# Kernel optimization log

Hardware: AMD Instinct MI355X
Metric: run time of the kernel (lower is better)

## Reference

```python
import jax, jax.numpy as jnp
import numpy as np

N, G, D, A = 131072, 256, 256, 64
NEG = -1e9
EPS = 1e-10


def segment_softmax(logits, idx, num_segments):
    # numerically stable softmax over ragged segments; works for [N] and [N, A]
    m = jax.ops.segment_max(logits, idx, num_segments=num_segments)
    e = jnp.exp(logits - m[idx])
    s = jax.ops.segment_sum(e, idx, num_segments=num_segments)
    return e / s[idx]


def setup_inputs() -> dict:
    key = jax.random.key(0)
    ks = jax.random.split(key, 12)
    values = jax.random.normal(ks[0], (N, D), dtype=jnp.float32)
    indices = jnp.sort(jax.random.randint(ks[1], (N,), 0, G))
    a_action = jax.random.randint(ks[2], (G,), 0, A)
    a_node = jax.random.randint(ks[3], (G,), 0, N)
    action_mask = jax.random.randint(ks[4], (G, A), 0, 2).astype(bool)
    n_nodes = jax.ops.segment_sum(jnp.ones((N,), jnp.int32), indices, num_segments=G)
    s = 0.02
    w_node = jax.random.normal(ks[5], (D,), dtype=jnp.float32) * s          # node_prob (no bias)
    W_agn = jax.random.normal(ks[6], (A, D), dtype=jnp.float32) * s         # action_given_node_prob
    b_agn = jnp.zeros((A,), jnp.float32)
    W_nga = jax.random.normal(ks[7], (A, D), dtype=jnp.float32) * s         # node_given_action_prob
    b_nga = jnp.zeros((A,), jnp.float32)
    W_qna = jax.random.normal(ks[8], (A, D), dtype=jnp.float32) * s         # q_node__action
    b_qna = jnp.zeros((A,), jnp.float32)
    W_qan = jax.random.normal(ks[9], (A, D), dtype=jnp.float32) * s         # q_action__node
    b_qan = jnp.zeros((A,), jnp.float32)
    return {"values": values, "indices": indices, "a_action": a_action, "a_node": a_node,
            "action_mask": action_mask, "n_nodes": n_nodes,
            "w_node": w_node, "W_agn": W_agn, "b_agn": b_agn, "W_nga": W_nga, "b_nga": b_nga,
            "W_qna": W_qna, "b_qna": b_qna, "W_qan": W_qan, "b_qan": b_qan}


def reference(values, indices, a_action, a_node, action_mask, n_nodes,
              w_node, W_agn, b_agn, W_nga, b_nga, W_qna, b_qna, W_qan, b_qan):
    n_g = action_mask.shape[0]
    segsum = lambda x: jax.ops.segment_sum(x, indices, num_segments=n_g)

    node_logits = values @ w_node                         # [N]
    agn_logits = values @ W_agn.T + b_agn                 # [N, A] action_given_node
    nga_logits = values @ W_nga.T + b_nga                 # [N, A] node_given_action
    mask_actions = action_mask[indices]                   # [N, A] per-node action validity

    # p(n) per graph, p(a|n) per node, p(a) per graph by marginalization
    p_n = segment_softmax(node_logits, indices, n_g)                       # [N]
    p_a_given_n = jax.nn.softmax(jnp.where(mask_actions, agn_logits, NEG), axis=-1)  # [N, A]
    p_a = segsum(p_n[:, None] * p_a_given_n)                               # [G, A]

    # masked p(n|a) used for eval (logprob/entropy)
    p_n_a_masked = segment_softmax(jnp.where(mask_actions, nga_logits, NEG), indices, n_g)  # [N, A]

    g_ar = jnp.arange(n_g)
    logprob = jnp.log(p_a[g_ar, a_action] + EPS) + jnp.log(p_n_a_masked[a_node, a_action] + EPS)  # [G]

    H_a = -jnp.sum(p_a * jnp.log(p_a + EPS), axis=-1)                      # [G]
    H_n_given_a = -segsum(p_n_a_masked * jnp.log(p_n_a_masked + EPS))      # [G, A]
    entropy = H_a + jnp.sum(p_a * H_n_given_a, axis=-1)                    # [G]

    # value estimate (unmasked p_n__a, as in f())
    p_n__a = segment_softmax(nga_logits, indices, n_g)                     # [N, A]
    q_a = segsum(values @ W_qan.T + b_qan)                                 # [G, A]
    q_n__a = values @ W_qna.T + b_qna                                      # [N, A]
    value = jnp.sum(p_a * (q_a + segsum(p_n__a * q_n__a)), axis=-1)        # [G]

    return (logprob, entropy, value, p_a, p_n__a)
```

## Files before the change

kernel.cpp:

```cpp
#include <hip/hip_runtime.h>
#include <hip/hip_bf16.h>

typedef unsigned short u16;
typedef unsigned int u32;
typedef __attribute__((ext_vector_type(4))) float f32x4;
typedef __attribute__((ext_vector_type(8))) short s16x8;
typedef __attribute__((ext_vector_type(8))) unsigned short u16x8;
typedef __attribute__((ext_vector_type(4))) unsigned short u16x4;

#define EPS_V (1e-10f)
#define TILES 4
#define NHALF (TILES * 4)

__device__ __forceinline__ u16 f2bf(float f) {
  unsigned u = __float_as_uint(f);
  u += 0x7fffu + ((u >> 16) & 1u);
  return (u16)(u >> 16);
}
__device__ __forceinline__ float bf2f(u16 h) {
  return __uint_as_float(((unsigned)h) << 16);
}
__device__ __forceinline__ float wred_sum(float v) {
#pragma unroll
  for (int o = 32; o; o >>= 1) v += __shfl_xor(v, o);
  return v;
}
__device__ __forceinline__ float red16(float v) {
  v += __shfl_xor(v, 1); v += __shfl_xor(v, 2);
  v += __shfl_xor(v, 4); v += __shfl_xor(v, 8);
  return v;
}
__device__ __forceinline__ bool mask_at(const void* m, int kind, int idx) {
  if (kind == 0) return ((const int*)m)[idx] != 0;
  if (kind == 1) return ((const float*)m)[idx] != 0.0f;
  return ((const unsigned char*)m)[idx] != 0;
}

__global__ __launch_bounds__(256) void k0_fused(
    const int* __restrict__ n_nodes, const unsigned int* __restrict__ mask_raw,
    const float* __restrict__ w_node, const float* __restrict__ W_agn,
    const float* __restrict__ W_nga, const float* __restrict__ W_qna,
    const float* __restrict__ W_qan,
    int* __restrict__ seg_start, int* __restrict__ mkind,
    float* __restrict__ zero_base, int nzero, u16* __restrict__ Wpack,
    int G, int ndw) {
  const int b = blockIdx.x;
  const int t = threadIdx.x;
  if (b == 0) {
    if (t < 64) {
      int base = t * 4;
      int v0 = (base + 0 < G) ? n_nodes[base + 0] : 0;
      int v1 = (base + 1 < G) ? n_nodes[base + 1] : 0;
      int v2 = (base + 2 < G) ? n_nodes[base + 2] : 0;
      int v3 = (base + 3 < G) ? n_nodes[base + 3] : 0;
      int lsum = v0 + v1 + v2 + v3;
      int x = lsum;
#pragma unroll
      for (int o = 1; o < 64; o <<= 1) {
        int y = __shfl_up(x, o);
        if (t >= o) x += y;
      }
      int run = x - lsum;
      if (base + 0 < G) seg_start[base + 0] = run; run += v0;
      if (base + 1 < G) seg_start[base + 1] = run; run += v1;
      if (base + 2 < G) seg_start[base + 2] = run; run += v2;
      if (base + 3 < G) seg_start[base + 3] = run; run += v3;
      if (t == 63) seg_start[G] = run;
    }
  } else if (b == 1) {
    __shared__ int notInt, notFloat;
    if (t == 0) { notInt = 0; notFloat = 0; }
    __syncthreads();
    int li = 0, lf = 0;
    for (int i = t; i < ndw; i += 256) {
      unsigned v = mask_raw[i];
      if (v != 0u && v != 1u) li = 1;
      if (v != 0u && v != 0x3F800000u) lf = 1;
    }
    if (li) atomicOr(&notInt, 1);
    if (lf) atomicOr(&notFloat, 1);
    __syncthreads();
    if (t == 0) mkind[0] = (!notInt) ? 0 : ((!notFloat) ? 1 : 2);
  } else if (b < 2 + 80) {
    int q = (b - 2) * 256 + t;
    int col = q >> 6, k = (q & 63) * 4;
    f32x4 v = (f32x4){0.f, 0.f, 0.f, 0.f};
    if (col < 64) v = *reinterpret_cast<const f32x4*>(W_agn + col * 256 + k);
    else if (col < 128) v = *reinterpret_cast<const f32x4*>(W_nga + (col - 64) * 256 + k);
    else if (col < 192) v = *reinterpret_cast<const f32x4*>(W_qna + (col - 128) * 256 + k);
    else if (col < 256) v = *reinterpret_cast<const f32x4*>(W_qan + (col - 192) * 256 + k);
    else if (col == 256) v = *reinterpret_cast<const f32x4*>(w_node + k);
    u16x4 h;
    h[0] = f2bf(v[0]); h[1] = f2bf(v[1]); h[2] = f2bf(v[2]); h[3] = f2bf(v[3]);
    *reinterpret_cast<u16x4*>(Wpack + (size_t)q * 4) = h;
  } else {
    int idx = (b - 82) * 256 + t;
    if (idx < nzero) zero_base[idx] = 0.f;
  }
}

__device__ __forceinline__ s16x8 frag_from_lds(const float* Vf, int m, int k0) {
  int g0 = ((k0 >> 2) ^ (m & 7));
  int g1 = g0 ^ 1;
  const f32x4 lo = *reinterpret_cast<const f32x4*>(&Vf[m * 256 + g0 * 4]);
  const f32x4 hi = *reinterpret_cast<const f32x4*>(&Vf[m * 256 + g1 * 4]);
  union { s16x8 v; u32 u[4]; } r;
  r.u[0] = __builtin_amdgcn_perm(__float_as_uint(lo[1]), __float_as_uint(lo[0]), 0x07060302u);
  r.u[1] = __builtin_amdgcn_perm(__float_as_uint(lo[3]), __float_as_uint(lo[2]), 0x07060302u);
  r.u[2] = __builtin_amdgcn_perm(__float_as_uint(hi[1]), __float_as_uint(hi[0]), 0x07060302u);
  r.u[3] = __builtin_amdgcn_perm(__float_as_uint(hi[3]), __float_as_uint(hi[2]), 0x07060302u);
  return r.v;
}

__global__ __launch_bounds__(256, 2) void k1_gemm(
    const float* __restrict__ values, const u16* __restrict__ Wpack,
    const int* __restrict__ indices, const void* __restrict__ mask,
    const int* __restrict__ mkind,
    const float* __restrict__ b_agn, const float* __restrict__ b_nga,
    const float* __restrict__ b_qna, const float* __restrict__ b_qan,
    u16* __restrict__ nga_bf, float* __restrict__ nga_f32,
    u16* __restrict__ qna, float* __restrict__ q_a,
    float* __restrict__ pa_un, float* __restrict__ Sn_at, int nga_is_bf) {
  __shared__ float ring[4][16 * 256];
  __shared__ u16 outbuf[2][16][68];
  __shared__ int segid[TILES * 64];

  const int t = threadIdx.x;
  const int lane = t & 63;
  const int wave = t >> 6;
  const int ln15 = lane & 15;
  const int kg = lane >> 4;
  const int blk0 = blockIdx.x * (TILES * 64);
  const int kind = mkind[0];

  s16x8 bfr[4][8];
  {
    const u16* wb = Wpack + (size_t)(wave * 64 + ln15) * 256 + kg * 8;
#pragma unroll
    for (int cg = 0; cg < 4; ++cg)
#pragma unroll
      for (int s = 0; s < 8; ++s)
        bfr[cg][s] = *reinterpret_cast<const s16x8*>(wb + (size_t)(cg * 16) * 256 + s * 32);
  }
  float bias_c[4];
  {
    const float* bp = (wave == 0) ? b_agn : (wave == 1) ? b_nga
                    : (wave == 2) ? b_qna : b_qan;
#pragma unroll
    for (int cg = 0; cg < 4; ++cg) bias_c[cg] = bp[cg * 16 + ln15];
  }
  s16x8 bn[8];
  if (wave == 0) {
    const u16* wb = Wpack + (size_t)(256 + ln15) * 256 + kg * 8;
#pragma unroll
    for (int s = 0; s < 8; ++s)
      bn[s] = *reinterpret_cast<const s16x8*>(wb + s * 32);
  }
  if (wave == 3) {
#pragma unroll
    for (int j = 0; j < 4; ++j)
      segid[lane + 64 * j] = indices[blk0 + lane + 64 * j];
  }
  float qpart[4] = {0.f, 0.f, 0.f, 0.f};
  int qg = (wave == 3) ? segid[kg * 4] : 0;
  float pa_[4] = {0.f, 0.f, 0.f, 0.f};
  float sn_ = 0.f;
  int pg = 0;
  bool mv[4] = {false, false, false, false};
  if (wave == 0) {
    pg = indices[blk0 + kg * 4];
#pragma unroll
    for (int cg = 0; cg < 4; ++cg)
      mv[cg] = mask_at(mask, kind, pg * 64 + cg * 16 + ln15);
  }

#define STAGE(hh)                                                              \
  {                                                                            \
    float* dst_ = ring[(hh) & 3];                                              \
    const int r0_ = blk0 + (hh) * 16;                                          \
    _Pragma("unroll")                                                          \
    for (int i_ = 0; i_ < 4; ++i_) {                                           \
      int m_ = wave * 4 + i_;                                                  \
      const float* gp_ = values + (size_t)(r0_ + m_) * 256 + ((lane ^ (m_ & 7)) << 2); \
      __builtin_amdgcn_global_load_lds(                                        \
          (const __attribute__((address_space(1))) void*)gp_,                  \
          (__attribute__((address_space(3))) void*)&dst_[m_ * 256], 16, 0, 0); \
    }                                                                          \
  }

  STAGE(0);
  STAGE(1);

  for (int h = 0; h < NHALF; ++h) {
    if (h + 2 < NHALF) STAGE(h + 2);
    if (h == 0) {
      asm volatile("s_waitcnt vmcnt(8) lgkmcnt(0)" ::: "memory");
    } else if (!nga_is_bf && wave == 1) {
      asm volatile("s_waitcnt vmcnt(0)" ::: "memory");
    } else if (h == NHALF - 1) {
      asm volatile("s_waitcnt vmcnt(0)" ::: "memory");
    } else if (h == NHALF - 2) {
      if (wave == 1 || wave == 2) asm volatile("s_waitcnt vmcnt(8)" ::: "memory");
      else                        asm volatile("s_waitcnt vmcnt(4)" ::: "memory");
    } else {
      if (wave == 1 || wave == 2) asm volatile("s_waitcnt vmcnt(12)" ::: "memory");
      else                        asm volatile("s_waitcnt vmcnt(8)" ::: "memory");
    }
    __builtin_amdgcn_sched_barrier(0);
    __builtin_amdgcn_s_barrier();
    __builtin_amdgcn_sched_barrier(0);

    const float* buf = ring[h & 3];
    const int row0 = blk0 + h * 16;

    f32x4 acc[4];
#pragma unroll
    for (int cg = 0; cg < 4; ++cg) acc[cg] = (f32x4){0.f, 0.f, 0.f, 0.f};
    f32x4 an0 = (f32x4){0.f, 0.f, 0.f, 0.f};

#pragma unroll
    for (int s = 0; s < 8; ++s) {
      const int k0 = s * 32 + kg * 8;
      s16x8 a0 = frag_from_lds(buf, ln15, k0);
#pragma unroll
      for (int cg = 0; cg < 4; ++cg)
        acc[cg] = __builtin_amdgcn_mfma_f32_16x16x32_bf16(a0, bfr[cg][s], acc[cg], 0, 0, 0);
      if (wave == 0)
        an0 = __builtin_amdgcn_mfma_f32_16x16x32_bf16(a0, bn[s], an0, 0, 0, 0);
    }

    if (wave == 0) {
#pragma unroll
      for (int r = 0; r < 4; ++r) {
        int m = kg * 4 + r;
        int g = segid[h * 16 + m];
        if (g != pg) {
#pragma unroll
          for (int cg = 0; cg < 4; ++cg) {
            atomicAdd(&pa_un[pg * 64 + cg * 16 + ln15], pa_[cg]);
            pa_[cg] = 0.f;
          }
          if (ln15 == 0) atomicAdd(&Sn_at[pg], sn_);
          sn_ = 0.f;
          pg = g;
#pragma unroll
          for (int cg = 0; cg < 4; ++cg)
            mv[cg] = mask_at(mask, kind, pg * 64 + cg * 16 + ln15);
        }
        float e0[4];
        float rs = 0.f;
#pragma unroll
        for (int cg = 0; cg < 4; ++cg) {
          e0[cg] = mv[cg] ? __expf(acc[cg][r] + bias_c[cg]) : 0.f;
          rs += e0[cg];
        }
        rs = red16(rs);
        float pn_e = __shfl(__expf(an0[r]), kg * 16);
        if (ln15 == 0) sn_ += pn_e;
        if (rs > 0.f) {
          float inv = pn_e / rs;
#pragma unroll
          for (int cg = 0; cg < 4; ++cg) pa_[cg] += e0[cg] * inv;
        } else {
#pragma unroll
          for (int cg = 0; cg < 4; ++cg) pa_[cg] += pn_e * 0.015625f;
        }
      }
    } else if (wave == 3) {
#pragma unroll
      for (int r = 0; r < 4; ++r) {
        int m = kg * 4 + r;
        int g = segid[h * 16 + m];
        if (g != qg) {
#pragma unroll
          for (int cg = 0; cg < 4; ++cg) {
            atomicAdd(&q_a[qg * 64 + cg * 16 + ln15], qpart[cg]);
            qpart[cg] = 0.f;
          }
          qg = g;
        }
#pragma unroll
        for (int cg = 0; cg < 4; ++cg)
          qpart[cg] += acc[cg][r] + bias_c[cg];
      }
    } else if (wave == 1 && !nga_is_bf) {
#pragma unroll
      for (int r = 0; r < 4; ++r)
#pragma unroll
        for (int cg = 0; cg < 4; ++cg)
          nga_f32[(size_t)(row0 + kg * 4 + r) * 64 + cg * 16 + ln15] = acc[cg][r] + bias_c[cg];
    } else {
#pragma unroll
      for (int r = 0; r < 4; ++r) {
        int m = kg * 4 + r;
#pragma unroll
        for (int cg = 0; cg < 4; ++cg)
          outbuf[wave - 1][m][cg * 16 + ln15] = f2bf(acc[cg][r] + bias_c[cg]);
      }
      u16* dstp = (wave == 1) ? nga_bf : qna;
#pragma unroll
      for (int j = 0; j < 4; ++j) {
        int li = lane + j * 64;
        int rr = li >> 4, cc = (li & 15) * 4;
        u16x4 v = *reinterpret_cast<const u16x4*>(&outbuf[wave - 1][rr][cc]);
        *reinterpret_cast<u16x4*>(dstp + (size_t)row0 * 64 + (size_t)li * 4) = v;
      }
    }
  }
#undef STAGE

  if (wave == 3) {
#pragma unroll
    for (int cg = 0; cg < 4; ++cg)
      atomicAdd(&q_a[qg * 64 + cg * 16 + ln15], qpart[cg]);
  }
  if (wave == 0) {
#pragma unroll
    for (int cg = 0; cg < 4; ++cg)
      atomicAdd(&pa_un[pg * 64 + cg * 16 + ln15], pa_[cg]);
    if (ln15 == 0) atomicAdd(&Sn_at[pg], sn_);
  }
}

__global__ __launch_bounds__(1024) void k2_segment(
    const u16* __restrict__ nga_bf, float* __restrict__ nga_f32,
    const u16* __restrict__ qna, const int* __restrict__ seg_start,
    const void* __restrict__ mask, const int* __restrict__ mkind,
    const float* __restrict__ q_a, const float* __restrict__ pa_un,
    const float* __restrict__ Sn_at,
    float* __restrict__ p_a, float* __restrict__ entropy, float* __restrict__ value,
    float* __restrict__ Su, float* __restrict__ pna, int nga_is_bf) {
  const int g = blockIdx.x;
  const int s = seg_start[g], e = seg_start[g + 1];
  const int n = e - s;
  const int t = threadIdx.x, lane = t & 63, wave = t >> 6;

  __shared__ float cs[16][64], cv[16][64], ci[16][64];
  __shared__ float sS[64];

  float s_u = 0.f, v_u = 0.f, i_u = 0.f;
  for (int i = s + wave; i < e; i += 16) {
    size_t base = (size_t)i * 64 + lane;
    float y = nga_is_bf ? bf2f(nga_bf[base]) : nga_f32[base];
    float ey = __expf(y);
    s_u += ey;
    v_u += ey * y;
    i_u += ey * bf2f(qna[base]);
  }
  cs[wave][lane] = s_u; cv[wave][lane] = v_u; ci[wave][lane] = i_u;
  __syncthreads();

  const int kind = mkind[0];
  if (t < 64) {
    int a = t;
    float S = 0.f, V = 0.f, I = 0.f;
#pragma unroll
    for (int w = 0; w < 16; ++w) { S += cs[w][a]; V += cv[w][a]; I += ci[w][a]; }
    float Sn = Sn_at[g];
    float P = (Sn > 0.f) ? pa_un[g * 64 + a] / Sn : 0.f;
    p_a[g * 64 + a] = P;
    Su[g * 64 + a] = S;
    sS[a] = (S > 0.f) ? 1.f / S : 0.f;
    float inner = (S > 0.f) ? I / S : 0.f;
    float Q = q_a[g * 64 + a];
    bool mva = mask_at(mask, kind, g * 64 + a);
    float Hn;
    if (n <= 0) Hn = 0.f;
    else if (!mva) Hn = -logf(1.0f / (float)n + EPS_V);
    else Hn = (S > 0.f) ? (logf(S) - V / S) : 0.f;
    float ent_c = -P * logf(P + EPS_V) + P * Hn;
    float val_c = P * (Q + inner);
    ent_c = wred_sum(ent_c);
    val_c = wred_sum(val_c);
    if (a == 0) { entropy[g] = ent_c; value[g] = val_c; }
  }
  __syncthreads();

  const int a0 = (t & 7) * 8;
  float is0 = sS[a0 + 0], is1 = sS[a0 + 1], is2 = sS[a0 + 2], is3 = sS[a0 + 3];
  float is4 = sS[a0 + 4], is5 = sS[a0 + 5], is6 = sS[a0 + 6], is7 = sS[a0 + 7];
  for (int i = s + (t >> 3); i < e; i += 128) {
    size_t base = (size_t)i * 64 + a0;
    float4 o0, o1;
    if (nga_is_bf) {
      u16x8 y = *reinterpret_cast<const u16x8*>(nga_bf + base);
      o0.x = __expf(bf2f(y[0])) * is0; o0.y = __expf(bf2f(y[1])) * is1;
      o0.z = __expf(bf2f(y[2])) * is2; o0.w = __expf(bf2f(y[3])) * is3;
      o1.x = __expf(bf2f(y[4])) * is4; o1.y = __expf(bf2f(y[5])) * is5;
      o1.z = __expf(bf2f(y[6])) * is6; o1.w = __expf(bf2f(y[7])) * is7;
    } else {
      const float4* src = reinterpret_cast<const float4*>(nga_f32 + base);
      float4 x0 = src[0], x1 = src[1];
      o0.x = __expf(x0.x) * is0; o0.y = __expf(x0.y) * is1;
      o0.z = __expf(x0.z) * is2; o0.w = __expf(x0.w) * is3;
      o1.x = __expf(x1.x) * is4; o1.y = __expf(x1.y) * is5;
      o1.z = __expf(x1.z) * is6; o1.w = __expf(x1.w) * is7;
    }
    float4* dst = reinterpret_cast<float4*>(pna + base);
    dst[0] = o0; dst[1] = o1;
  }
}

__global__ __launch_bounds__(256) void k3_logprob(
    const float* __restrict__ p_a, const u16* __restrict__ nga_bf,
    const float* __restrict__ nga_f32, const int* __restrict__ indices,
    const int* __restrict__ a_action, const int* __restrict__ a_node,
    const void* __restrict__ mask, const int* __restrict__ mkind,
    const int* __restrict__ n_nodes, const float* __restrict__ Su,
    float* __restrict__ logprob, int G, int nga_is_bf) {
  int g = blockIdx.x * blockDim.x + threadIdx.x;
  if (g >= G) return;
  int kind = mkind[0];
  int a = a_action[g];
  float t1 = logf(p_a[g * 64 + a] + EPS_V);
  int node = a_node[g];
  int g2 = indices[node];
  float p2;
  if (mask_at(mask, kind, g2 * 64 + a)) {
    float S = Su[g2 * 64 + a];
    float y = nga_is_bf ? bf2f(nga_bf[(size_t)node * 64 + a]) : nga_f32[(size_t)node * 64 + a];
    p2 = (S > 0.f) ? __expf(y) / S : 0.f;
  } else {
    p2 = 1.0f / (float)n_nodes[g2];
  }
  logprob[g] = t1 + logf(p2 + EPS_V);
}

extern "C" void kernel_launch(void* const* d_in, const int* in_sizes, int n_in,
                              void* d_out, int out_size, void* d_ws, size_t ws_size,
                              hipStream_t stream) {
  const float* values = (const float*)d_in[0];
  const int* indices = (const int*)d_in[1];
  const int* a_action = (const int*)d_in[2];
  const int* a_node = (const int*)d_in[3];
  const void* action_mask = d_in[4];
  const int* n_nodes = (const int*)d_in[5];
  const float* w_node = (const float*)d_in[6];
  const float* W_agn = (const float*)d_in[7];
  const float* b_agn = (const float*)d_in[8];
  const float* W_nga = (const float*)d_in[9];
  const float* b_nga = (const float*)d_in[10];
  const float* W_qna = (const float*)d_in[11];
  const float* b_qna = (const float*)d_in[12];
  const float* W_qan = (const float*)d_in[13];
  const float* b_qan = (const float*)d_in[14];

  const int N = in_sizes[1];
  const int G = in_sizes[2];
  const int GA = in_sizes[4];

  float* out = (float*)d_out;
  float* o_logprob = out;
  float* o_entropy = out + G;
  float* o_value = out + 2 * G;
  float* o_pa = out + 3 * G;
  float* o_pna = out + 3 * G + GA;

  char* w = (char*)d_ws;
  size_t off = 0;
  u16* qna = (u16*)(w + off); off += (size_t)N * 64 * 2;
  float* Su = (float*)(w + off); off += (size_t)GA * 4;
  float* zero_base = (float*)(w + off);
  float* q_a = (float*)(w + off); off += (size_t)GA * 4;
  float* pa_un = (float*)(w + off); off += (size_t)GA * 4;
  float* Sn_at = (float*)(w + off); off += (size_t)G * 4;
  int nzero = 2 * GA + G;
  int* seg_start = (int*)(w + off); off += (size_t)(G + 1) * 4;
  int* mkind = (int*)(w + off); off += 256;
  off = (off + 255) & ~(size_t)255;
  u16* Wpack = (u16*)(w + off); off += (size_t)320 * 256 * 2;
  u16* nga_bf = (u16*)(w + off);
  size_t need_bf = off + (size_t)N * 64 * 2;
  int nga_is_bf = (ws_size >= need_bf) ? 1 : 0;
  float* nga_f32 = o_pna;

  int zero_blocks = (nzero + 255) / 256;
  k0_fused<<<2 + 80 + zero_blocks, 256, 0, stream>>>(
      n_nodes, (const unsigned int*)action_mask, w_node, W_agn, W_nga, W_qna, W_qan,
      seg_start, mkind, zero_base, nzero, Wpack, G, GA / 4);
  k1_gemm<<<N / (TILES * 64), 256, 0, stream>>>(
      values, Wpack, indices, action_mask, mkind,
      b_agn, b_nga, b_qna, b_qan,
      nga_bf, nga_f32, qna, q_a, pa_un, Sn_at, nga_is_bf);
  k2_segment<<<G, 1024, 0, stream>>>(nga_bf, nga_f32, qna, seg_start,
                                     action_mask, mkind, q_a, pa_un, Sn_at,
                                     o_pa, o_entropy, o_value, Su, o_pna, nga_is_bf);
  k3_logprob<<<(G + 255) / 256, 256, 0, stream>>>(
      o_pa, nga_bf, nga_f32, indices, a_action, a_node,
      action_mask, mkind, n_nodes, Su, o_logprob, G, nga_is_bf);
}
```

Before: 95.52 us.

## Fuse segment softmax reductions into GEMM epilogue and drop qna intermediate

The GEMM kernel now computes exp(nga), the segment sums S and V, and the q-weighted sum I directly in its epilogue, accumulating them per segment with atomics. Wave 1 shares the exp values with wave 2 through LDS, and wave 2 processes them one tile late. This removes the bf16 qna buffer write and re-read, and removes the first reduction pass of the segment kernel. In exchange it adds more atomics, extra LDS traffic, and more work and waits inside the GEMM loop.

Result: slower. 124.8 us (+30.6%).

```diff
diff --git a/kernel.cpp b/kernel.cpp
--- a/kernel.cpp
+++ b/kernel.cpp
@@ -119,10 +119,12 @@
     const float* __restrict__ b_agn, const float* __restrict__ b_nga,
     const float* __restrict__ b_qna, const float* __restrict__ b_qan,
     u16* __restrict__ nga_bf, float* __restrict__ nga_f32,
-    u16* __restrict__ qna, float* __restrict__ q_a,
-    float* __restrict__ pa_un, float* __restrict__ Sn_at, int nga_is_bf) {
+    float* __restrict__ q_a, float* __restrict__ pa_un,
+    float* __restrict__ Sn_at, float* __restrict__ S_at,
+    float* __restrict__ V_at, float* __restrict__ I_at, int nga_is_bf) {
   __shared__ float ring[4][16 * 256];
-  __shared__ u16 outbuf[2][16][68];
+  __shared__ u16 outbuf[16][68];
+  __shared__ float e_lds[2][16][68];
   __shared__ int segid[TILES * 64];
 
   const int t = threadIdx.x;
@@ -167,11 +169,23 @@
   float sn_ = 0.f;
   int pg = 0;
   bool mv[4] = {false, false, false, false};
+  float Ss_[4] = {0.f, 0.f, 0.f, 0.f};
+  float Vv_[4] = {0.f, 0.f, 0.f, 0.f};
+  int sg = 0;
+  float Ii_[4] = {0.f, 0.f, 0.f, 0.f};
+  int ig = 0;
+  f32x4 pacc[4];
+#pragma unroll
+  for (int cg = 0; cg < 4; ++cg) pacc[cg] = (f32x4){0.f, 0.f, 0.f, 0.f};
   if (wave == 0) {
     pg = indices[blk0 + kg * 4];
 #pragma unroll
     for (int cg = 0; cg < 4; ++cg)
       mv[cg] = mask_at(mask, kind, pg * 64 + cg * 16 + ln15);
+  } else if (wave == 1) {
+    sg = indices[blk0 + kg * 4];
+  } else if (wave == 2) {
+    ig = indices[blk0 + kg * 4];
   }
 
 #define STAGE(hh)                                                              \
@@ -196,15 +210,15 @@
     if (h == 0) {
       asm volatile("s_waitcnt vmcnt(8) lgkmcnt(0)" ::: "memory");
     } else if (!nga_is_bf && wave == 1) {
-      asm volatile("s_waitcnt vmcnt(0)" ::: "memory");
+      asm volatile("s_waitcnt vmcnt(0) lgkmcnt(0)" ::: "memory");
     } else if (h == NHALF - 1) {
-      asm volatile("s_waitcnt vmcnt(0)" ::: "memory");
+      asm volatile("s_waitcnt vmcnt(0) lgkmcnt(0)" ::: "memory");
     } else if (h == NHALF - 2) {
-      if (wave == 1 || wave == 2) asm volatile("s_waitcnt vmcnt(8)" ::: "memory");
-      else                        asm volatile("s_waitcnt vmcnt(4)" ::: "memory");
+      if (wave == 1) asm volatile("s_waitcnt vmcnt(8) lgkmcnt(0)" ::: "memory");
+      else           asm volatile("s_waitcnt vmcnt(4)" ::: "memory");
     } else {
-      if (wave == 1 || wave == 2) asm volatile("s_waitcnt vmcnt(12)" ::: "memory");
-      else                        asm volatile("s_waitcnt vmcnt(8)" ::: "memory");
+      if (wave == 1) asm volatile("s_waitcnt vmcnt(12) lgkmcnt(0)" ::: "memory");
+      else           asm volatile("s_waitcnt vmcnt(8)" ::: "memory");
     }
     __builtin_amdgcn_sched_barrier(0);
     __builtin_amdgcn_s_barrier();
@@ -266,7 +280,63 @@
           for (int cg = 0; cg < 4; ++cg) pa_[cg] += pn_e * 0.015625f;
         }
       }
-    } else if (wave == 3) {
+    } else if (wave == 1) {
+#pragma unroll
+      for (int r = 0; r < 4; ++r) {
+        int m = kg * 4 + r;
+        int g = segid[h * 16 + m];
+        if (g != sg) {
+#pragma unroll
+          for (int cg = 0; cg < 4; ++cg) {
+            atomicAdd(&S_at[sg * 64 + cg * 16 + ln15], Ss_[cg]);
+            atomicAdd(&V_at[sg * 64 + cg * 16 + ln15], Vv_[cg]);
+            Ss_[cg] = 0.f; Vv_[cg] = 0.f;
+          }
+          sg = g;
+        }
+#pragma unroll
+        for (int cg = 0; cg < 4; ++cg) {
+          float y = acc[cg][r] + bias_c[cg];
+          float e = __expf(y);
+          e_lds[h & 1][m][cg * 16 + ln15] = e;
+          Ss_[cg] += e;
+          Vv_[cg] += e * y;
+          if (nga_is_bf) outbuf[m][cg * 16 + ln15] = f2bf(y);
+          else nga_f32[(size_t)(row0 + m) * 64 + cg * 16 + ln15] = y;
+        }
+      }
+      if (nga_is_bf) {
+#pragma unroll
+        for (int j = 0; j < 4; ++j) {
+          int li = lane + j * 64;
+          int rr = li >> 4, cc = (li & 15) * 4;
+          u16x4 v = *reinterpret_cast<const u16x4*>(&outbuf[rr][cc]);
+          *reinterpret_cast<u16x4*>(nga_bf + (size_t)row0 * 64 + (size_t)li * 4) = v;
+        }
+      }
+    } else if (wave == 2) {
+      if (h > 0) {
+        const int hp = h - 1;
+#pragma unroll
+        for (int r = 0; r < 4; ++r) {
+          int m = kg * 4 + r;
+          int g = segid[hp * 16 + m];
+          if (g != ig) {
+#pragma unroll
+            for (int cg = 0; cg < 4; ++cg) {
+              atomicAdd(&I_at[ig * 64 + cg * 16 + ln15], Ii_[cg]);
+              Ii_[cg] = 0.f;
+            }
+            ig = g;
+          }
+#pragma unroll
+          for (int cg = 0; cg < 4; ++cg)
+            Ii_[cg] += e_lds[hp & 1][m][cg * 16 + ln15] * (pacc[cg][r] + bias_c[cg]);
+        }
+      }
+#pragma unroll
+      for (int cg = 0; cg < 4; ++cg) pacc[cg] = acc[cg];
+    } else {
 #pragma unroll
       for (int r = 0; r < 4; ++r) {
         int m = kg * 4 + r;
@@ -283,79 +353,76 @@
         for (int cg = 0; cg < 4; ++cg)
           qpart[cg] += acc[cg][r] + bias_c[cg];
       }
-    } else if (wave == 1 && !nga_is_bf) {
-#pragma unroll
-      for (int r = 0; r < 4; ++r)
-#pragma unroll
-        for (int cg = 0; cg < 4; ++cg)
-          nga_f32[(size_t)(row0 + kg * 4 + r) * 64 + cg * 16 + ln15] = acc[cg][r] + bias_c[cg];
-    } else {
-#pragma unroll
-      for (int r = 0; r < 4; ++r) {
-        int m = kg * 4 + r;
-#pragma unroll
-        for (int cg = 0; cg < 4; ++cg)
-          outbuf[wave - 1][m][cg * 16 + ln15] = f2bf(acc[cg][r] + bias_c[cg]);
-      }
-      u16* dstp = (wave == 1) ? nga_bf : qna;
-#pragma unroll
-      for (int j = 0; j < 4; ++j) {
-        int li = lane + j * 64;
-        int rr = li >> 4, cc = (li & 15) * 4;
-        u16x4 v = *reinterpret_cast<const u16x4*>(&outbuf[wave - 1][rr][cc]);
-        *reinterpret_cast<u16x4*>(dstp + (size_t)row0 * 64 + (size_t)li * 4) = v;
-      }
     }
   }
 #undef STAGE
 
-  if (wave == 3) {
-#pragma unroll
-    for (int cg = 0; cg < 4; ++cg)
-      atomicAdd(&q_a[qg * 64 + cg * 16 + ln15], qpart[cg]);
-  }
+  asm volatile("s_waitcnt lgkmcnt(0)" ::: "memory");
+  __builtin_amdgcn_sched_barrier(0);
+  __builtin_amdgcn_s_barrier();
+  __builtin_amdgcn_sched_barrier(0);
+
   if (wave == 0) {
 #pragma unroll
     for (int cg = 0; cg < 4; ++cg)
       atomicAdd(&pa_un[pg * 64 + cg * 16 + ln15], pa_[cg]);
     if (ln15 == 0) atomicAdd(&Sn_at[pg], sn_);
+  } else if (wave == 1) {
+#pragma unroll
+    for (int cg = 0; cg < 4; ++cg) {
+      atomicAdd(&S_at[sg * 64 + cg * 16 + ln15], Ss_[cg]);
+      atomicAdd(&V_at[sg * 64 + cg * 16 + ln15], Vv_[cg]);
+    }
+  } else if (wave == 2) {
+    const int hp = NHALF - 1;
+#pragma unroll
+    for (int r = 0; r < 4; ++r) {
+      int m = kg * 4 + r;
+      int g = segid[hp * 16 + m];
+      if (g != ig) {
+#pragma unroll
+        for (int cg = 0; cg < 4; ++cg) {
+          atomicAdd(&I_at[ig * 64 + cg * 16 + ln15], Ii_[cg]);
+          Ii_[cg] = 0.f;
+        }
+        ig = g;
+      }
+#pragma unroll
+      for (int cg = 0; cg < 4; ++cg)
+        Ii_[cg] += e_lds[hp & 1][m][cg * 16 + ln15] * (pacc[cg][r] + bias_c[cg]);
+    }
+#pragma unroll
+    for (int cg = 0; cg < 4; ++cg)
+      atomicAdd(&I_at[ig * 64 + cg * 16 + ln15], Ii_[cg]);
+  } else {
+#pragma unroll
+    for (int cg = 0; cg < 4; ++cg)
+      atomicAdd(&q_a[qg * 64 + cg * 16 + ln15], qpart[cg]);
   }
 }
 
 __global__ __launch_bounds__(1024) void k2_segment(
     const u16* __restrict__ nga_bf, float* __restrict__ nga_f32,
-    const u16* __restrict__ qna, const int* __restrict__ seg_start,
-    const void* __restrict__ mask, const int* __restrict__ mkind,
+    const int* __restrict__ seg_start, const void* __restrict__ mask,
+    const int* __restrict__ mkind,
     const float* __restrict__ q_a, const float* __restrict__ pa_un,
-    const float* __restrict__ Sn_at,
+    const float* __restrict__ Sn_at, const float* __restrict__ S_at,
+    const float* __restrict__ V_at, const float* __restrict__ I_at,
+    const int* __restrict__ n_nodes,
     float* __restrict__ p_a, float* __restrict__ entropy, float* __restrict__ value,
     float* __restrict__ Su, float* __restrict__ pna, int nga_is_bf) {
   const int g = blockIdx.x;
   const int s = seg_start[g], e = seg_start[g + 1];
-  const int n = e - s;
-  const int t = threadIdx.x, lane = t & 63, wave = t >> 6;
-
-  __shared__ float cs[16][64], cv[16][64], ci[16][64];
+  const int t = threadIdx.x;
+
   __shared__ float sS[64];
 
-  float s_u = 0.f, v_u = 0.f, i_u = 0.f;
-  for (int i = s + wave; i < e; i += 16) {
-    size_t base = (size_t)i * 64 + lane;
-    float y = nga_is_bf ? bf2f(nga_bf[base]) : nga_f32[base];
-    float ey = __expf(y);
-    s_u += ey;
-    v_u += ey * y;
-    i_u += ey * bf2f(qna[base]);
-  }
-  cs[wave][lane] = s_u; cv[wave][lane] = v_u; ci[wave][lane] = i_u;
-  __syncthreads();
-
-  const int kind = mkind[0];
   if (t < 64) {
     int a = t;
-    float S = 0.f, V = 0.f, I = 0.f;
-#pragma unroll
-    for (int w = 0; w < 16; ++w) { S += cs[w][a]; V += cv[w][a]; I += ci[w][a]; }
+    int n = n_nodes[g];
+    float S = S_at[g * 64 + a];
+    float V = V_at[g * 64 + a];
+    float I = I_at[g * 64 + a];
     float Sn = Sn_at[g];
     float P = (Sn > 0.f) ? pa_un[g * 64 + a] / Sn : 0.f;
     p_a[g * 64 + a] = P;
@@ -363,7 +430,7 @@
     sS[a] = (S > 0.f) ? 1.f / S : 0.f;
     float inner = (S > 0.f) ? I / S : 0.f;
     float Q = q_a[g * 64 + a];
-    bool mva = mask_at(mask, kind, g * 64 + a);
+    bool mva = mask_at(mask, mkind[0], g * 64 + a);
     float Hn;
     if (n <= 0) Hn = 0.f;
     else if (!mva) Hn = -logf(1.0f / (float)n + EPS_V);
@@ -458,13 +525,15 @@
 
   char* w = (char*)d_ws;
   size_t off = 0;
-  u16* qna = (u16*)(w + off); off += (size_t)N * 64 * 2;
   float* Su = (float*)(w + off); off += (size_t)GA * 4;
   float* zero_base = (float*)(w + off);
   float* q_a = (float*)(w + off); off += (size_t)GA * 4;
   float* pa_un = (float*)(w + off); off += (size_t)GA * 4;
+  float* S_at = (float*)(w + off); off += (size_t)GA * 4;
+  float* V_at = (float*)(w + off); off += (size_t)GA * 4;
+  float* I_at = (float*)(w + off); off += (size_t)GA * 4;
   float* Sn_at = (float*)(w + off); off += (size_t)G * 4;
-  int nzero = 2 * GA + G;
+  int nzero = 5 * GA + G;
   int* seg_start = (int*)(w + off); off += (size_t)(G + 1) * 4;
   int* mkind = (int*)(w + off); off += 256;
   off = (off + 255) & ~(size_t)255;
@@ -481,9 +550,10 @@
   k1_gemm<<<N / (TILES * 64), 256, 0, stream>>>(
       values, Wpack, indices, action_mask, mkind,
       b_agn, b_nga, b_qna, b_qan,
-      nga_bf, nga_f32, qna, q_a, pa_un, Sn_at, nga_is_bf);
-  k2_segment<<<G, 1024, 0, stream>>>(nga_bf, nga_f32, qna, seg_start,
+      nga_bf, nga_f32, q_a, pa_un, Sn_at, S_at, V_at, I_at, nga_is_bf);
+  k2_segment<<<G, 1024, 0, stream>>>(nga_bf, nga_f32, seg_start,
                                      action_mask, mkind, q_a, pa_un, Sn_at,
+                                     S_at, V_at, I_at, n_nodes,
                                      o_pa, o_entropy, o_value, Su, o_pna, nga_is_bf);
   k3_logprob<<<(G + 255) / 256, 256, 0, stream>>>(
       o_pa, nga_bf, nga_f32, indices, a_action, a_node,
```
